# Kernel optimization log

Measured on AMD Instinct MI355X. Metric: run time of the kernel, lower is better.

## Reference

```python
import jax, jax.numpy as jnp
import numpy as np

B, C, T = 128, 23, 2000
N_FFT, HOP = 200, 100
NFREQ = N_FFT // 2 + 1        # 101
FT = 1 + (T - N_FFT) // HOP   # 19 time frames per channel
EMB, HEADS, DEPTH = 256, 8, 4
DH = EMB // HEADS             # 32 head dim
FF = 4 * EMB                  # 1024 ffn hidden
MASK_RATIO = 0.15


def _posenc(n, d):
    pos = np.arange(n)[:, None].astype(np.float32)
    div = np.exp(np.arange(0, d, 2).astype(np.float32) * -(np.log(10000.0) / d))
    pe = np.zeros((n, d), np.float32)
    pe[:, 0::2] = np.sin(pos * div)
    pe[:, 1::2] = np.cos(pos * div)
    return jnp.asarray(pe)


def _stft_mag(sig):
    # sig: (..., T) -> (..., FT, NFREQ); rectangular window, center=False, onesided
    idx = np.arange(FT)[:, None] * HOP + np.arange(N_FFT)[None, :]
    frames = sig[..., idx]                      # (..., FT, N_FFT)
    return jnp.abs(jnp.fft.rfft(frames, axis=-1))


def _layernorm(x, g, b):
    mu = x.mean(-1, keepdims=True)
    var = x.var(-1, keepdims=True)
    return (x - mu) / jnp.sqrt(var + 1e-5) * g + b


def setup_inputs() -> dict:
    key = jax.random.key(0)
    ks = jax.random.split(key, 12)
    inp = {
        'x': jax.random.normal(ks[0], (B, C, T), jnp.float32),
        'mask': jax.random.uniform(ks[1], (B, C, T)) < MASK_RATIO,
        'n_channel_offset': 0,
        'W_proj': jax.random.normal(ks[2], (NFREQ, EMB), jnp.float32) / np.sqrt(NFREQ),
        'b_proj': jnp.zeros((EMB,), jnp.float32),
        'channel_tokens': jax.random.normal(ks[3], (C, EMB), jnp.float32),
        'ln1_g': jnp.ones((DEPTH, EMB), jnp.float32),
        'ln1_b': jnp.zeros((DEPTH, EMB), jnp.float32),
        'Wq': jax.random.normal(ks[4], (DEPTH, EMB, EMB), jnp.float32) / np.sqrt(EMB),
        'Wk': jax.random.normal(ks[5], (DEPTH, EMB, EMB), jnp.float32) / np.sqrt(EMB),
        'Wv': jax.random.normal(ks[6], (DEPTH, EMB, EMB), jnp.float32) / np.sqrt(EMB),
        'Wo': jax.random.normal(ks[7], (DEPTH, EMB, EMB), jnp.float32) / np.sqrt(EMB),
        'ln2_g': jnp.ones((DEPTH, EMB), jnp.float32),
        'ln2_b': jnp.zeros((DEPTH, EMB), jnp.float32),
        'W1': jax.random.normal(ks[8], (DEPTH, EMB, FF), jnp.float32) / np.sqrt(EMB),
        'b1': jnp.zeros((DEPTH, FF), jnp.float32),
        'W2': jax.random.normal(ks[9], (DEPTH, FF, EMB), jnp.float32) / np.sqrt(FF),
        'b2': jnp.zeros((DEPTH, EMB), jnp.float32),
    }
    return inp


def reference(x, mask, n_channel_offset, W_proj, b_proj, channel_tokens,
              ln1_g, ln1_b, Wq, Wk, Wv, Wo, ln2_g, ln2_b, W1, b1, W2, b2):
    xm = jnp.where(mask, 0.0, x)
    # STFT magnitude for all channels at once: (B, C, FT, NFREQ)
    spec_c = _stft_mag(x)
    spec_m = _stft_mag(xm)
    # patch-frequency linear embedding -> (B, C, FT, EMB)
    emb_c = spec_c @ W_proj + b_proj
    emb_m = spec_m @ W_proj + b_proj
    tok = jnp.take(channel_tokens, jnp.arange(C) + n_channel_offset, axis=0)
    pe = _posenc(FT, EMB)
    emb_c = emb_c + tok[None, :, None, :] + pe[None, None, :, :]
    emb_m = emb_m + tok[None, :, None, :] + pe[None, None, :, :]
    S = C * FT
    emb_c = emb_c.reshape(B, S, EMB)
    h = emb_m.reshape(B, S, EMB)

    scale = DH ** -0.5
    for l in range(DEPTH):
        # linear attention block (prenorm)
        hn = _layernorm(h, ln1_g[l], ln1_b[l])
        q = (hn @ Wq[l]).reshape(B, S, HEADS, DH).transpose(0, 2, 1, 3)
        k = (hn @ Wk[l]).reshape(B, S, HEADS, DH).transpose(0, 2, 1, 3)
        v = (hn @ Wv[l]).reshape(B, S, HEADS, DH).transpose(0, 2, 1, 3)
        q = jax.nn.softmax(q, axis=-1) * scale   # softmax over feature dim
        k = jax.nn.softmax(k, axis=-2)           # softmax over sequence dim
        ctx = jnp.einsum('bhsd,bhse->bhde', k, v)      # (B,H,DH,DH)
        attn = jnp.einsum('bhsd,bhde->bhse', q, ctx)   # (B,H,S,DH)
        attn = attn.transpose(0, 2, 1, 3).reshape(B, S, EMB)
        h = h + attn @ Wo[l]
        # feed-forward block (prenorm)
        hn = _layernorm(h, ln2_g[l], ln2_b[l])
        h = h + jax.nn.gelu(hn @ W1[l] + b1[l]) @ W2[l] + b2[l]
    return (emb_c, h)
```

## Files before the change

kernel.cpp:

```cpp
#include <hip/hip_runtime.h>
#include <math.h>

#define BB 128
#define CC 23
#define TT 2000
#define NFFT 200
#define HOP 100
#define NFREQ 101
#define FTW 19
#define EMB 256
#define HEADS 8
#define DH 32
#define FFD 1024
#define DEPTH 4
#define SS (CC*FTW)
#define NROWS (BB*SS)
#define ROWT 16

typedef __attribute__((ext_vector_type(8))) short bf16x8;
typedef __attribute__((ext_vector_type(4))) float f32x4;
#define MFMA16 __builtin_amdgcn_mfma_f32_16x16x32_bf16

__device__ inline unsigned short f2bf(float f) {
    unsigned u = __float_as_uint(f);
    unsigned r = (u + 0x7FFFu + ((u >> 16) & 1u)) >> 16;
    return (unsigned short)r;
}
__device__ inline float bf2f(unsigned short s) {
    return __uint_as_float(((unsigned)s) << 16);
}
__device__ inline bf16x8 ld_frag(const unsigned short* p) {
    union { uint4 u; bf16x8 f; } v;
    v.u = *(const uint4*)p;
    return v.f;
}

__global__ __launch_bounds__(256) void k_init(float* pe) {
    int i = blockIdx.x * 256 + threadIdx.x;
    if (i < FTW * (EMB / 2)) {
        int t = i / (EMB / 2), j = i % (EMB / 2);
        float dv = expf((-9.210340371976184f / (float)EMB) * (float)(2 * j));
        float a = (float)t * dv;
        pe[t * EMB + 2 * j]     = sinf(a);
        pe[t * EMB + 2 * j + 1] = cosf(a);
    }
}

__global__ __launch_bounds__(256) void k_binit(unsigned short* Bt) {
    int i = blockIdx.x * 256 + threadIdx.x;
    if (i >= 256 * 224) return;
    int n = i / 224, k = i - (i / 224) * 224;
    int fq = ((n >> 5) << 4) + (n & 15);
    int kind = (n >> 4) & 1;
    float v = 0.f;
    if (k < 200 && fq < 101) {
        int kn = (fq * k) % 200;
        float th = 6.283185307179586f * (float)kn / 200.f;
        v = kind ? sinf(th) : cosf(th);
    }
    Bt[n * 224 + k] = f2bf(v);
}

__global__ __launch_bounds__(256) void k_tr(const float* __restrict__ in, unsigned short* __restrict__ out,
                                            int K, int N, size_t inStride, size_t outStride) {
    __shared__ float t[32][33];
    int k0 = blockIdx.y * 32, n0 = blockIdx.x * 32;
    const float* ip = in + blockIdx.z * inStride;
    unsigned short* op = out + blockIdx.z * outStride;
    int tx = threadIdx.x & 31, ty = threadIdx.x >> 5;
#pragma unroll
    for (int i = 0; i < 32; i += 8)
        t[ty + i][tx] = ip[(size_t)(k0 + ty + i) * N + n0 + tx];
    __syncthreads();
#pragma unroll
    for (int i = 0; i < 32; i += 8)
        op[(size_t)(n0 + ty + i) * K + k0 + tx] = f2bf(t[tx][ty + i]);
}

__global__ __launch_bounds__(256, 2) void k_stft(const float* __restrict__ x,
                                                 const int* __restrict__ mask,
                                                 const unsigned short* __restrict__ Bt,
                                                 float* __restrict__ specc,
                                                 float* __restrict__ specm) {
    int masked = blockIdx.y;
    int r0 = blockIdx.x * 64;
    __shared__ unsigned short aT[64 * 232];
    for (int t = threadIdx.x; t < 64 * 29; t += 256) {
        int row = t / 29;
        int ch = t - row * 29;
        int col0 = ch * 8;
        union { uint4 u; unsigned short s[8]; } pk;
        if (col0 < 200) {
            int fr = r0 + row;
            int bc = fr / 19, f = fr - bc * 19;
            const float* src = x + (size_t)bc * TT + f * HOP + col0;
            float4 v0 = *(const float4*)src;
            float4 v1 = *(const float4*)(src + 4);
            if (masked) {
                const int* ms = mask + (size_t)bc * TT + f * HOP + col0;
                int4 m0 = *(const int4*)ms;
                int4 m1 = *(const int4*)(ms + 4);
                if (m0.x) v0.x = 0.f; if (m0.y) v0.y = 0.f; if (m0.z) v0.z = 0.f; if (m0.w) v0.w = 0.f;
                if (m1.x) v1.x = 0.f; if (m1.y) v1.y = 0.f; if (m1.z) v1.z = 0.f; if (m1.w) v1.w = 0.f;
            }
            pk.s[0] = f2bf(v0.x); pk.s[1] = f2bf(v0.y); pk.s[2] = f2bf(v0.z); pk.s[3] = f2bf(v0.w);
            pk.s[4] = f2bf(v1.x); pk.s[5] = f2bf(v1.y); pk.s[6] = f2bf(v1.z); pk.s[7] = f2bf(v1.w);
        } else {
            pk.u = (uint4){0, 0, 0, 0};
        }
        *(uint4*)&aT[row * 232 + col0] = pk.u;
    }
    __syncthreads();
    int lane = threadIdx.x & 63, w = threadIdx.x >> 6;
    int m16 = lane & 15, q = lane >> 4;
    f32x4 acc[4][4];
#pragma unroll
    for (int mt = 0; mt < 4; mt++)
#pragma unroll
        for (int nt = 0; nt < 4; nt++) acc[mt][nt] = (f32x4){0.f, 0.f, 0.f, 0.f};
    for (int kk = 0; kk < 7; kk++) {
        int k0 = kk * 32 + q * 8;
        bf16x8 af[4], bfr[4];
#pragma unroll
        for (int mt = 0; mt < 4; mt++) af[mt] = ld_frag(&aT[(mt * 16 + m16) * 232 + k0]);
#pragma unroll
        for (int nt = 0; nt < 4; nt++) bfr[nt] = ld_frag(&Bt[(w * 64 + nt * 16 + m16) * 224 + k0]);
#pragma unroll
        for (int mt = 0; mt < 4; mt++)
#pragma unroll
            for (int nt = 0; nt < 4; nt++) acc[mt][nt] = MFMA16(af[mt], bfr[nt], acc[mt][nt], 0, 0, 0);
    }
    float* out = masked ? specm : specc;
#pragma unroll
    for (int pt = 0; pt < 2; pt++) {
        int fq = w * 32 + pt * 16 + m16;
        if (fq < NFREQ) {
#pragma unroll
            for (int mt = 0; mt < 4; mt++)
#pragma unroll
                for (int r = 0; r < 4; r++) {
                    float re = acc[mt][pt * 2][r];
                    float im = acc[mt][pt * 2 + 1][r];
                    int row = mt * 16 + q * 4 + r;
                    out[(size_t)(r0 + row) * NFREQ + fq] = sqrtf(re * re + im * im);
                }
        }
    }
}

__global__ __launch_bounds__(256) void k_proj(const float* __restrict__ spec,
                                              const float* __restrict__ Wp,
                                              const float* __restrict__ bp,
                                              const float* __restrict__ tok,
                                              const int* __restrict__ offp,
                                              const float* __restrict__ pe,
                                              float* __restrict__ out) {
    int r0 = blockIdx.x * ROWT;
    __shared__ float sp[ROWT][NFREQ];
    for (int i = threadIdx.x; i < ROWT * NFREQ; i += 256) {
        int r = i / NFREQ, kk = i % NFREQ;
        sp[r][kk] = spec[(size_t)(r0 + r) * NFREQ + kk];
    }
    __syncthreads();
    int j = threadIdx.x;
    float acc[ROWT];
#pragma unroll
    for (int r = 0; r < ROWT; r++) acc[r] = 0.f;
    for (int kk = 0; kk < NFREQ; kk++) {
        float w = Wp[kk * EMB + j];
#pragma unroll
        for (int r = 0; r < ROWT; r++) acc[r] += sp[r][kk] * w;
    }
    int off = *offp;
    float bj = bp[j];
#pragma unroll
    for (int r = 0; r < ROWT; r++) {
        int g = r0 + r;
        int c = (g / FTW) % CC;
        int f = g % FTW;
        out[(size_t)g * EMB + j] = acc[r] + bj + tok[(c + off) * EMB + j] + pe[f * EMB + j];
    }
}

__device__ inline void ln_stage8(const float* __restrict__ h, int r0,
                                 const float* __restrict__ g, const float* __restrict__ b,
                                 unsigned short* aT) {
    int row = threadIdx.x >> 3, part = threadIdx.x & 7;
    const float* hr = h + (size_t)(r0 + row) * EMB + part * 32;
    float s1 = 0.f, s2 = 0.f;
#pragma unroll
    for (int i = 0; i < 8; i++) {
        float4 v = *(const float4*)(hr + i * 4);
        s1 += v.x + v.y + v.z + v.w;
        s2 += v.x * v.x + v.y * v.y + v.z * v.z + v.w * v.w;
    }
    s1 += __shfl_xor(s1, 1); s1 += __shfl_xor(s1, 2); s1 += __shfl_xor(s1, 4);
    s2 += __shfl_xor(s2, 1); s2 += __shfl_xor(s2, 2); s2 += __shfl_xor(s2, 4);
    float mu = s1 * (1.f / EMB);
    float var = s2 * (1.f / EMB) - mu * mu;
    float rstd = rsqrtf(var + 1e-5f);
    const float* gp = g + part * 32;
    const float* bp = b + part * 32;
#pragma unroll
    for (int i = 0; i < 4; i++) {
        float4 va = *(const float4*)(hr + i * 8);
        float4 vb = *(const float4*)(hr + i * 8 + 4);
        float4 ga = *(const float4*)(gp + i * 8);
        float4 gb = *(const float4*)(gp + i * 8 + 4);
        float4 ba = *(const float4*)(bp + i * 8);
        float4 bb = *(const float4*)(bp + i * 8 + 4);
        union { uint4 u; unsigned short s[8]; } pk;
        pk.s[0] = f2bf((va.x - mu) * rstd * ga.x + ba.x);
        pk.s[1] = f2bf((va.y - mu) * rstd * ga.y + ba.y);
        pk.s[2] = f2bf((va.z - mu) * rstd * ga.z + ba.z);
        pk.s[3] = f2bf((va.w - mu) * rstd * ga.w + ba.w);
        pk.s[4] = f2bf((vb.x - mu) * rstd * gb.x + bb.x);
        pk.s[5] = f2bf((vb.y - mu) * rstd * gb.y + bb.y);
        pk.s[6] = f2bf((vb.z - mu) * rstd * gb.z + bb.z);
        pk.s[7] = f2bf((vb.w - mu) * rstd * gb.w + bb.w);
        *(uint4*)&aT[row * 264 + part * 32 + i * 8] = pk.u;
    }
}

__global__ __launch_bounds__(512, 4) void k_qkv(const float* __restrict__ h,
                                                const float* __restrict__ lng,
                                                const float* __restrict__ lnb,
                                                const unsigned short* __restrict__ Wt,
                                                unsigned short* __restrict__ qb,
                                                unsigned short* __restrict__ kb,
                                                unsigned short* __restrict__ vb) {
    __shared__ unsigned short aT[64 * 264];
    __shared__ unsigned short ob[64 * 264];
    int r0 = blockIdx.x * 64;
    ln_stage8(h, r0, lng, lnb, aT);
    __syncthreads();
    int lane = threadIdx.x & 63, w = threadIdx.x >> 6;
    int m16 = lane & 15, q = lane >> 4;
    f32x4 acc[4][2];

    auto do_gemm = [&](int gg) {
        int cb = gg * 256 + w * 32;
#pragma unroll
        for (int mt = 0; mt < 4; mt++)
#pragma unroll
            for (int nt = 0; nt < 2; nt++) acc[mt][nt] = (f32x4){0.f, 0.f, 0.f, 0.f};
        bf16x8 bc0 = ld_frag(&Wt[(size_t)(cb + m16) * EMB + q * 8]);
        bf16x8 bc1 = ld_frag(&Wt[(size_t)(cb + 16 + m16) * EMB + q * 8]);
        for (int kk = 0; kk < 8; kk++) {
            int k0 = kk * 32 + q * 8;
            bf16x8 bn0, bn1;
            if (kk < 7) {
                bn0 = ld_frag(&Wt[(size_t)(cb + m16) * EMB + k0 + 32]);
                bn1 = ld_frag(&Wt[(size_t)(cb + 16 + m16) * EMB + k0 + 32]);
            }
            bf16x8 af[4];
#pragma unroll
            for (int mt = 0; mt < 4; mt++) af[mt] = ld_frag(&aT[(mt * 16 + m16) * 264 + k0]);
#pragma unroll
            for (int mt = 0; mt < 4; mt++) acc[mt][0] = MFMA16(af[mt], bc0, acc[mt][0], 0, 0, 0);
#pragma unroll
            for (int mt = 0; mt < 4; mt++) acc[mt][1] = MFMA16(af[mt], bc1, acc[mt][1], 0, 0, 0);
            bc0 = bn0; bc1 = bn1;
        }
    };

    do_gemm(0);
    for (int gg = 0; gg < 3; gg++) {
        __syncthreads();
#pragma unroll
        for (int nt = 0; nt < 2; nt++)
#pragma unroll
            for (int mt = 0; mt < 4; mt++)
#pragma unroll
                for (int r = 0; r < 4; r++)
                    ob[(mt * 16 + q * 4 + r) * 264 + w * 32 + nt * 16 + m16] = f2bf(acc[mt][nt][r]);
        __syncthreads();
        unsigned short* dst = (gg == 0) ? qb : (gg == 1) ? kb : vb;
        for (int t = threadIdx.x; t < 2048; t += 512) {
            int row = t >> 5, c8 = (t & 31) * 8;
            *(uint4*)&dst[(size_t)(r0 + row) * EMB + c8] = *(uint4*)&ob[row * 264 + c8];
        }
        if (gg < 2) do_gemm(gg + 1);
    }
}

__global__ __launch_bounds__(256) void k_kctx(const unsigned short* __restrict__ kb,
                                              const unsigned short* __restrict__ vb,
                                              float* __restrict__ ctx) {
    int b = blockIdx.x >> 3, h = blockIdx.x & 7;
    int d = threadIdx.x & 31, g = threadIdx.x >> 5;
    size_t colbase = (size_t)b * SS * EMB + h * DH;
    __shared__ float red[8][32];
    __shared__ float kmax[32], krs[32];
    float mx = -1e30f;
    for (int s = g; s < SS; s += 8) mx = fmaxf(mx, bf2f(kb[colbase + (size_t)s * EMB + d]));
    red[g][d] = mx;
    __syncthreads();
    if (threadIdx.x < 32) {
        mx = red[0][d];
        for (int i = 1; i < 8; i++) mx = fmaxf(mx, red[i][d]);
        kmax[d] = mx;
    }
    __syncthreads();
    mx = kmax[d];
    float sm = 0.f;
    for (int s = g; s < SS; s += 8) sm += __expf(bf2f(kb[colbase + (size_t)s * EMB + d]) - mx);
    __syncthreads();
    red[g][d] = sm;
    __syncthreads();
    if (threadIdx.x < 32) {
        sm = 0.f;
        for (int i = 0; i < 8; i++) sm += red[i][d];
        krs[d] = 1.f / sm;
    }
    __syncthreads();
    int e = threadIdx.x & 31, db = threadIdx.x >> 5;
    float acc[4] = {0.f, 0.f, 0.f, 0.f};
    __shared__ float ksm[8][32], vls[8][32];
    float kmd = kmax[d], krd = krs[d];
    for (int s0 = 0; s0 < SS; s0 += 8) {
        int s = s0 + g;
        float kvv = 0.f, vvv = 0.f;
        if (s < SS) {
            kvv = __expf(bf2f(kb[colbase + (size_t)s * EMB + d]) - kmd) * krd;
            vvv = bf2f(vb[colbase + (size_t)s * EMB + d]);
        }
        __syncthreads();
        ksm[g][d] = kvv;
        vls[g][d] = vvv;
        __syncthreads();
#pragma unroll
        for (int ssx = 0; ssx < 8; ssx++) {
            float vv = vls[ssx][e];
#pragma unroll
            for (int i = 0; i < 4; i++) acc[i] += ksm[ssx][db * 4 + i] * vv;
        }
    }
#pragma unroll
    for (int i = 0; i < 4; i++)
        ctx[((size_t)b * HEADS + h) * 1024 + e * 32 + (db * 4 + i)] = acc[i];
}

__global__ __launch_bounds__(256, 4) void k_attn_o(const unsigned short* __restrict__ qb,
                                                   const float* __restrict__ ctxT,
                                                   const unsigned short* __restrict__ WoT,
                                                   float* __restrict__ h) {
    int b = blockIdx.x, s0 = blockIdx.y * 16;
    __shared__ unsigned short qsmb[16 * 264];
    __shared__ unsigned short ctxb[8 * 32 * 48];
    __shared__ unsigned short atb[16 * 264];
    int j = threadIdx.x;
    for (int idx = j; idx < 8192; idx += 256) {
        int hh = idx >> 10, rem = idx & 1023, e = rem >> 5, d = rem & 31;
        ctxb[hh * (32 * 48) + e * 48 + d] = f2bf(ctxT[(size_t)b * 8192 + idx]);
    }
    const float scale = 0.17677669529663687f;
    for (int r = 0; r < 16; r++) {
        int s = s0 + r; if (s > SS - 1) s = SS - 1;
        float v = bf2f(qb[((size_t)b * SS + s) * EMB + j]);
        float mxv = v;
#pragma unroll
        for (int m = 1; m < 32; m <<= 1) mxv = fmaxf(mxv, __shfl_xor(mxv, m));
        float ex = __expf(v - mxv);
        float sm = ex;
#pragma unroll
        for (int m = 1; m < 32; m <<= 1) sm += __shfl_xor(sm, m);
        qsmb[r * 264 + j] = f2bf(ex / sm * scale);
    }
    __syncthreads();
    int lane = threadIdx.x & 63, w = threadIdx.x >> 6;
    int m16 = lane & 15, q = lane >> 4;
#pragma unroll
    for (int hi = 0; hi < 2; hi++) {
        int head = w * 2 + hi;
        bf16x8 af = ld_frag(&qsmb[m16 * 264 + head * 32 + q * 8]);
#pragma unroll
        for (int half = 0; half < 2; half++) {
            bf16x8 bfr = ld_frag(&ctxb[head * (32 * 48) + (half * 16 + m16) * 48 + q * 8]);
            f32x4 acc = (f32x4){0.f, 0.f, 0.f, 0.f};
            acc = MFMA16(af, bfr, acc, 0, 0, 0);
#pragma unroll
            for (int r = 0; r < 4; r++)
                atb[(q * 4 + r) * 264 + head * 32 + half * 16 + m16] = f2bf(acc[r]);
        }
    }
    __syncthreads();
    f32x4 acc2[4];
#pragma unroll
    for (int nt = 0; nt < 4; nt++) acc2[nt] = (f32x4){0.f, 0.f, 0.f, 0.f};
    for (int kk = 0; kk < 8; kk++) {
        int k0 = kk * 32 + q * 8;
        bf16x8 af = ld_frag(&atb[m16 * 264 + k0]);
#pragma unroll
        for (int nt = 0; nt < 4; nt++) {
            bf16x8 bfr = ld_frag(&WoT[(size_t)(w * 64 + nt * 16 + m16) * EMB + k0]);
            acc2[nt] = MFMA16(af, bfr, acc2[nt], 0, 0, 0);
        }
    }
#pragma unroll
    for (int nt = 0; nt < 4; nt++) {
        int c = w * 64 + nt * 16 + m16;
#pragma unroll
        for (int r = 0; r < 4; r++) {
            int s = s0 + q * 4 + r;
            if (s < SS) h[((size_t)b * SS + s) * EMB + c] += acc2[nt][r];
        }
    }
}

__global__ __launch_bounds__(512, 4) void k_ffn(const float* __restrict__ hin,
                                                const float* __restrict__ lng,
                                                const float* __restrict__ lnb,
                                                const unsigned short* __restrict__ W1T,
                                                const float* __restrict__ b1,
                                                const unsigned short* __restrict__ W2T,
                                                const float* __restrict__ b2,
                                                float* __restrict__ h) {
    __shared__ unsigned short aT[64 * 264];
    __shared__ unsigned short fch[64 * 264];
    int r0 = blockIdx.x * 64;
    ln_stage8(hin, r0, lng, lnb, aT);
    __syncthreads();
    int lane = threadIdx.x & 63, w = threadIdx.x >> 6;
    int m16 = lane & 15, q = lane >> 4;
    f32x4 acc2[4][2];
#pragma unroll
    for (int mt = 0; mt < 4; mt++)
#pragma unroll
        for (int nt = 0; nt < 2; nt++) acc2[mt][nt] = (f32x4){0.f, 0.f, 0.f, 0.f};
    f32x4 accf[4][2];

    auto gemm1 = [&](int ch) {
        int cb = ch * 256 + w * 32;
#pragma unroll
        for (int mt = 0; mt < 4; mt++)
#pragma unroll
            for (int nt = 0; nt < 2; nt++) accf[mt][nt] = (f32x4){0.f, 0.f, 0.f, 0.f};
        bf16x8 bc0 = ld_frag(&W1T[(size_t)(cb + m16) * EMB + q * 8]);
        bf16x8 bc1 = ld_frag(&W1T[(size_t)(cb + 16 + m16) * EMB + q * 8]);
        for (int kk = 0; kk < 8; kk++) {
            int k0 = kk * 32 + q * 8;
            bf16x8 bn0, bn1;
            if (kk < 7) {
                bn0 = ld_frag(&W1T[(size_t)(cb + m16) * EMB + k0 + 32]);
                bn1 = ld_frag(&W1T[(size_t)(cb + 16 + m16) * EMB + k0 + 32]);
            }
            bf16x8 af[4];
#pragma unroll
            for (int mt = 0; mt < 4; mt++) af[mt] = ld_frag(&aT[(mt * 16 + m16) * 264 + k0]);
#pragma unroll
            for (int mt = 0; mt < 4; mt++) accf[mt][0] = MFMA16(af[mt], bc0, accf[mt][0], 0, 0, 0);
#pragma unroll
            for (int mt = 0; mt < 4; mt++) accf[mt][1] = MFMA16(af[mt], bc1, accf[mt][1], 0, 0, 0);
            bc0 = bn0; bc1 = bn1;
        }
    };

    gemm1(0);
    for (int ch = 0; ch < 4; ch++) {
        __syncthreads();
#pragma unroll
        for (int nt = 0; nt < 2; nt++) {
            int cl = w * 32 + nt * 16 + m16;
            float bias = b1[ch * 256 + cl];
#pragma unroll
            for (int mt = 0; mt < 4; mt++)
#pragma unroll
                for (int r = 0; r < 4; r++) {
                    float xv = accf[mt][nt][r] + bias;
                    float z = 0.7978845608028654f * (xv + 0.044715f * xv * xv * xv);
                    z = fminf(fmaxf(z, -15.f), 15.f);
                    float t = __expf(2.f * z);
                    float gl = 0.5f * xv * (1.f + (t - 1.f) / (t + 1.f));
                    fch[(mt * 16 + q * 4 + r) * 264 + cl] = f2bf(gl);
                }
        }
        __syncthreads();
        {
            int rb = w * 32;
            bf16x8 bc0 = ld_frag(&W2T[(size_t)(rb + m16) * FFD + ch * 256 + q * 8]);
            bf16x8 bc1 = ld_frag(&W2T[(size_t)(rb + 16 + m16) * FFD + ch * 256 + q * 8]);
            for (int kk = 0; kk < 8; kk++) {
                int k0 = kk * 32 + q * 8;
                bf16x8 bn0, bn1;
                if (kk < 7) {
                    bn0 = ld_frag(&W2T[(size_t)(rb + m16) * FFD + ch * 256 + k0 + 32]);
                    bn1 = ld_frag(&W2T[(size_t)(rb + 16 + m16) * FFD + ch * 256 + k0 + 32]);
                }
                bf16x8 af[4];
#pragma unroll
                for (int mt = 0; mt < 4; mt++) af[mt] = ld_frag(&fch[(mt * 16 + m16) * 264 + k0]);
#pragma unroll
                for (int mt = 0; mt < 4; mt++) acc2[mt][0] = MFMA16(af[mt], bc0, acc2[mt][0], 0, 0, 0);
#pragma unroll
                for (int mt = 0; mt < 4; mt++) acc2[mt][1] = MFMA16(af[mt], bc1, acc2[mt][1], 0, 0, 0);
                bc0 = bn0; bc1 = bn1;
            }
        }
        if (ch < 3) gemm1(ch + 1);
    }
#pragma unroll
    for (int nt = 0; nt < 2; nt++) {
        int c = w * 32 + nt * 16 + m16;
        float bias = b2[c];
#pragma unroll
        for (int mt = 0; mt < 4; mt++)
#pragma unroll
            for (int r = 0; r < 4; r++)
                h[(size_t)(r0 + mt * 16 + q * 4 + r) * EMB + c] += acc2[mt][nt][r] + bias;
    }
}

extern "C" void kernel_launch(void* const* d_in, const int* in_sizes, int n_in,
                              void* d_out, int out_size, void* d_ws, size_t ws_size,
                              hipStream_t stream) {
    const float* x    = (const float*)d_in[0];
    const int* mask   = (const int*)d_in[1];
    const int* offp   = (const int*)d_in[2];
    const float* Wp   = (const float*)d_in[3];
    const float* bp   = (const float*)d_in[4];
    const float* tok  = (const float*)d_in[5];
    const float* ln1g = (const float*)d_in[6];
    const float* ln1b = (const float*)d_in[7];
    const float* Wq   = (const float*)d_in[8];
    const float* Wk   = (const float*)d_in[9];
    const float* Wv   = (const float*)d_in[10];
    const float* Wo   = (const float*)d_in[11];
    const float* ln2g = (const float*)d_in[12];
    const float* ln2b = (const float*)d_in[13];
    const float* W1   = (const float*)d_in[14];
    const float* b1   = (const float*)d_in[15];
    const float* W2   = (const float*)d_in[16];
    const float* b2   = (const float*)d_in[17];

    float* out_embc = (float*)d_out;
    float* h = out_embc + (size_t)NROWS * EMB;

    char* base = (char*)d_ws;
    float* pe = (float*)base;
    unsigned short* Bt = (unsigned short*)(base + 19712);
    unsigned short* wT = (unsigned short*)(base + 134400);
    unsigned short* qb = (unsigned short*)(base + 6425856);
    unsigned short* kb = qb + (size_t)NROWS * EMB;
    unsigned short* vb = kb + (size_t)NROWS * EMB;
    float* specc = (float*)qb;
    float* specm = specc + (size_t)NROWS * NFREQ;
    float* ctxT = (float*)(base + 6425856 + 3ull * NROWS * EMB * 2);

    unsigned short* WqkvT = wT;
    unsigned short* WoT   = wT + 786432;
    unsigned short* W1T   = WoT + 262144;
    unsigned short* W2T   = W1T + 1048576;

    k_init<<<10, 256, 0, stream>>>(pe);
    k_binit<<<224, 256, 0, stream>>>(Bt);
    k_tr<<<dim3(8, 8, 4), 256, 0, stream>>>(Wq, WqkvT + 0,      256, 256, 65536, 196608);
    k_tr<<<dim3(8, 8, 4), 256, 0, stream>>>(Wk, WqkvT + 65536,  256, 256, 65536, 196608);
    k_tr<<<dim3(8, 8, 4), 256, 0, stream>>>(Wv, WqkvT + 131072, 256, 256, 65536, 196608);
    k_tr<<<dim3(8, 8, 4), 256, 0, stream>>>(Wo, WoT, 256, 256, 65536, 65536);
    k_tr<<<dim3(32, 8, 4), 256, 0, stream>>>(W1, W1T, 256, 1024, 262144, 262144);
    k_tr<<<dim3(8, 32, 4), 256, 0, stream>>>(W2, W2T, 1024, 256, 262144, 262144);

    k_stft<<<dim3(NROWS / 64, 2), 256, 0, stream>>>(x, mask, Bt, specc, specm);
    k_proj<<<NROWS / ROWT, 256, 0, stream>>>(specc, Wp, bp, tok, offp, pe, out_embc);
    k_proj<<<NROWS / ROWT, 256, 0, stream>>>(specm, Wp, bp, tok, offp, pe, h);

    for (int l = 0; l < DEPTH; l++) {
        k_qkv<<<NROWS / 64, 512, 0, stream>>>(h, ln1g + l * EMB, ln1b + l * EMB,
                                              WqkvT + (size_t)l * 196608, qb, kb, vb);
        k_kctx<<<BB * HEADS, 256, 0, stream>>>(kb, vb, ctxT);
        k_attn_o<<<dim3(BB, (SS + 15) / 16), 256, 0, stream>>>(qb, ctxT, WoT + (size_t)l * 65536, h);
        k_ffn<<<NROWS / 64, 512, 0, stream>>>(h, ln2g + l * EMB, ln2b + l * EMB,
                                              W1T + (size_t)l * 262144, b1 + (size_t)l * FFD,
                                              W2T + (size_t)l * 262144, b2 + (size_t)l * EMB, h);
    }
}
```

Before: 2.153 ms.

## Halve chunk width in QKV and FFN kernels to cut LDS and registers

The QKV and FFN kernels now process output columns in 128-wide chunks instead of 256-wide ones. That halves the staging LDS buffer and the per-wave accumulator registers, and launch bounds are raised from 4 to 6 blocks per CU so more blocks can be resident. The activation row stride is also padded from 264 to 280 to change the LDS bank mapping. The cost is twice as many sync/epilogue rounds, and each B fragment is reused across fewer MFMAs, so global weight loads per FLOP go up.

```diff
diff --git a/kernel.cpp b/kernel.cpp
--- a/kernel.cpp
+++ b/kernel.cpp
@@ -16,6 +16,8 @@
 #define SS (CC*FTW)
 #define NROWS (BB*SS)
 #define ROWT 16
+#define ATS 280
+#define FCS 136
 
 typedef __attribute__((ext_vector_type(8))) short bf16x8;
 typedef __attribute__((ext_vector_type(4))) float f32x4;
@@ -218,69 +220,60 @@
         pk.s[5] = f2bf((vb.y - mu) * rstd * gb.y + bb.y);
         pk.s[6] = f2bf((vb.z - mu) * rstd * gb.z + bb.z);
         pk.s[7] = f2bf((vb.w - mu) * rstd * gb.w + bb.w);
-        *(uint4*)&aT[row * 264 + part * 32 + i * 8] = pk.u;
-    }
-}
-
-__global__ __launch_bounds__(512, 4) void k_qkv(const float* __restrict__ h,
+        *(uint4*)&aT[row * ATS + part * 32 + i * 8] = pk.u;
+    }
+}
+
+__global__ __launch_bounds__(512, 6) void k_qkv(const float* __restrict__ h,
                                                 const float* __restrict__ lng,
                                                 const float* __restrict__ lnb,
                                                 const unsigned short* __restrict__ Wt,
                                                 unsigned short* __restrict__ qb,
                                                 unsigned short* __restrict__ kb,
                                                 unsigned short* __restrict__ vb) {
-    __shared__ unsigned short aT[64 * 264];
-    __shared__ unsigned short ob[64 * 264];
+    __shared__ unsigned short aT[64 * ATS];
+    __shared__ unsigned short ob[64 * FCS];
     int r0 = blockIdx.x * 64;
     ln_stage8(h, r0, lng, lnb, aT);
     __syncthreads();
     int lane = threadIdx.x & 63, w = threadIdx.x >> 6;
     int m16 = lane & 15, q = lane >> 4;
-    f32x4 acc[4][2];
+    f32x4 acc[4];
 
     auto do_gemm = [&](int gg) {
-        int cb = gg * 256 + w * 32;
-#pragma unroll
-        for (int mt = 0; mt < 4; mt++)
-#pragma unroll
-            for (int nt = 0; nt < 2; nt++) acc[mt][nt] = (f32x4){0.f, 0.f, 0.f, 0.f};
-        bf16x8 bc0 = ld_frag(&Wt[(size_t)(cb + m16) * EMB + q * 8]);
-        bf16x8 bc1 = ld_frag(&Wt[(size_t)(cb + 16 + m16) * EMB + q * 8]);
+        int cb = gg * 128 + w * 16;
+#pragma unroll
+        for (int mt = 0; mt < 4; mt++) acc[mt] = (f32x4){0.f, 0.f, 0.f, 0.f};
+        bf16x8 bc = ld_frag(&Wt[(size_t)(cb + m16) * EMB + q * 8]);
         for (int kk = 0; kk < 8; kk++) {
             int k0 = kk * 32 + q * 8;
-            bf16x8 bn0, bn1;
-            if (kk < 7) {
-                bn0 = ld_frag(&Wt[(size_t)(cb + m16) * EMB + k0 + 32]);
-                bn1 = ld_frag(&Wt[(size_t)(cb + 16 + m16) * EMB + k0 + 32]);
-            }
+            bf16x8 bn;
+            if (kk < 7) bn = ld_frag(&Wt[(size_t)(cb + m16) * EMB + k0 + 32]);
             bf16x8 af[4];
 #pragma unroll
-            for (int mt = 0; mt < 4; mt++) af[mt] = ld_frag(&aT[(mt * 16 + m16) * 264 + k0]);
-#pragma unroll
-            for (int mt = 0; mt < 4; mt++) acc[mt][0] = MFMA16(af[mt], bc0, acc[mt][0], 0, 0, 0);
-#pragma unroll
-            for (int mt = 0; mt < 4; mt++) acc[mt][1] = MFMA16(af[mt], bc1, acc[mt][1], 0, 0, 0);
-            bc0 = bn0; bc1 = bn1;
+            for (int mt = 0; mt < 4; mt++) af[mt] = ld_frag(&aT[(mt * 16 + m16) * ATS + k0]);
+#pragma unroll
+            for (int mt = 0; mt < 4; mt++) acc[mt] = MFMA16(af[mt], bc, acc[mt], 0, 0, 0);
+            bc = bn;
         }
     };
 
     do_gemm(0);
-    for (int gg = 0; gg < 3; gg++) {
+    for (int gg = 0; gg < 6; gg++) {
         __syncthreads();
 #pragma unroll
-        for (int nt = 0; nt < 2; nt++)
-#pragma unroll
-            for (int mt = 0; mt < 4; mt++)
-#pragma unroll
-                for (int r = 0; r < 4; r++)
-                    ob[(mt * 16 + q * 4 + r) * 264 + w * 32 + nt * 16 + m16] = f2bf(acc[mt][nt][r]);
+        for (int mt = 0; mt < 4; mt++)
+#pragma unroll
+            for (int r = 0; r < 4; r++)
+                ob[(mt * 16 + q * 4 + r) * FCS + w * 16 + m16] = f2bf(acc[mt][r]);
         __syncthreads();
-        unsigned short* dst = (gg == 0) ? qb : (gg == 1) ? kb : vb;
-        for (int t = threadIdx.x; t < 2048; t += 512) {
-            int row = t >> 5, c8 = (t & 31) * 8;
-            *(uint4*)&dst[(size_t)(r0 + row) * EMB + c8] = *(uint4*)&ob[row * 264 + c8];
-        }
-        if (gg < 2) do_gemm(gg + 1);
+        unsigned short* dst = (gg < 2) ? qb : (gg < 4) ? kb : vb;
+        int cc0 = (gg & 1) * 128;
+        for (int t = threadIdx.x; t < 1024; t += 512) {
+            int row = t >> 4, c8 = (t & 15) * 8;
+            *(uint4*)&dst[(size_t)(r0 + row) * EMB + cc0 + c8] = *(uint4*)&ob[row * FCS + c8];
+        }
+        if (gg < 5) do_gemm(gg + 1);
     }
 }
 
@@ -408,7 +401,7 @@
     }
 }
 
-__global__ __launch_bounds__(512, 4) void k_ffn(const float* __restrict__ hin,
+__global__ __launch_bounds__(512, 6) void k_ffn(const float* __restrict__ hin,
                                                 const float* __restrict__ lng,
                                                 const float* __restrict__ lnb,
                                                 const unsigned short* __restrict__ W1T,
@@ -416,8 +409,8 @@
                                                 const unsigned short* __restrict__ W2T,
                                                 const float* __restrict__ b2,
                                                 float* __restrict__ h) {
-    __shared__ unsigned short aT[64 * 264];
-    __shared__ unsigned short fch[64 * 264];
+    __shared__ unsigned short aT[64 * ATS];
+    __shared__ unsigned short fch[64 * FCS];
     int r0 = blockIdx.x * 64;
     ln_stage8(hin, r0, lng, lnb, aT);
     __syncthreads();
@@ -428,68 +421,58 @@
     for (int mt = 0; mt < 4; mt++)
 #pragma unroll
         for (int nt = 0; nt < 2; nt++) acc2[mt][nt] = (f32x4){0.f, 0.f, 0.f, 0.f};
-    f32x4 accf[4][2];
+    f32x4 acc1[4];
 
     auto gemm1 = [&](int ch) {
-        int cb = ch * 256 + w * 32;
-#pragma unroll
-        for (int mt = 0; mt < 4; mt++)
-#pragma unroll
-            for (int nt = 0; nt < 2; nt++) accf[mt][nt] = (f32x4){0.f, 0.f, 0.f, 0.f};
-        bf16x8 bc0 = ld_frag(&W1T[(size_t)(cb + m16) * EMB + q * 8]);
-        bf16x8 bc1 = ld_frag(&W1T[(size_t)(cb + 16 + m16) * EMB + q * 8]);
+        int cb = ch * 128 + w * 16;
+#pragma unroll
+        for (int mt = 0; mt < 4; mt++) acc1[mt] = (f32x4){0.f, 0.f, 0.f, 0.f};
+        bf16x8 bc = ld_frag(&W1T[(size_t)(cb + m16) * EMB + q * 8]);
         for (int kk = 0; kk < 8; kk++) {
             int k0 = kk * 32 + q * 8;
-            bf16x8 bn0, bn1;
-            if (kk < 7) {
-                bn0 = ld_frag(&W1T[(size_t)(cb + m16) * EMB + k0 + 32]);
-                bn1 = ld_frag(&W1T[(size_t)(cb + 16 + m16) * EMB + k0 + 32]);
-            }
+            bf16x8 bn;
+            if (kk < 7) bn = ld_frag(&W1T[(size_t)(cb + m16) * EMB + k0 + 32]);
             bf16x8 af[4];
 #pragma unroll
-            for (int mt = 0; mt < 4; mt++) af[mt] = ld_frag(&aT[(mt * 16 + m16) * 264 + k0]);
-#pragma unroll
-            for (int mt = 0; mt < 4; mt++) accf[mt][0] = MFMA16(af[mt], bc0, accf[mt][0], 0, 0, 0);
-#pragma unroll
-            for (int mt = 0; mt < 4; mt++) accf[mt][1] = MFMA16(af[mt], bc1, accf[mt][1], 0, 0, 0);
-            bc0 = bn0; bc1 = bn1;
+            for (int mt = 0; mt < 4; mt++) af[mt] = ld_frag(&aT[(mt * 16 + m16) * ATS + k0]);
+#pragma unroll
+            for (int mt = 0; mt < 4; mt++) acc1[mt] = MFMA16(af[mt], bc, acc1[mt], 0, 0, 0);
+            bc = bn;
         }
     };
 
     gemm1(0);
-    for (int ch = 0; ch < 4; ch++) {
+    for (int ch = 0; ch < 8; ch++) {
         __syncthreads();
-#pragma unroll
-        for (int nt = 0; nt < 2; nt++) {
-            int cl = w * 32 + nt * 16 + m16;
-            float bias = b1[ch * 256 + cl];
+        {
+            float bias = b1[ch * 128 + w * 16 + m16];
 #pragma unroll
             for (int mt = 0; mt < 4; mt++)
 #pragma unroll
                 for (int r = 0; r < 4; r++) {
-                    float xv = accf[mt][nt][r] + bias;
+                    float xv = acc1[mt][r] + bias;
                     float z = 0.7978845608028654f * (xv + 0.044715f * xv * xv * xv);
                     z = fminf(fmaxf(z, -15.f), 15.f);
                     float t = __expf(2.f * z);
                     float gl = 0.5f * xv * (1.f + (t - 1.f) / (t + 1.f));
-                    fch[(mt * 16 + q * 4 + r) * 264 + cl] = f2bf(gl);
+                    fch[(mt * 16 + q * 4 + r) * FCS + w * 16 + m16] = f2bf(gl);
                 }
         }
         __syncthreads();
         {
             int rb = w * 32;
-            bf16x8 bc0 = ld_frag(&W2T[(size_t)(rb + m16) * FFD + ch * 256 + q * 8]);
-            bf16x8 bc1 = ld_frag(&W2T[(size_t)(rb + 16 + m16) * FFD + ch * 256 + q * 8]);
-            for (int kk = 0; kk < 8; kk++) {
+            bf16x8 bc0 = ld_frag(&W2T[(size_t)(rb + m16) * FFD + ch * 128 + q * 8]);
+            bf16x8 bc1 = ld_frag(&W2T[(size_t)(rb + 16 + m16) * FFD + ch * 128 + q * 8]);
+            for (int kk = 0; kk < 4; kk++) {
                 int k0 = kk * 32 + q * 8;
                 bf16x8 bn0, bn1;
-                if (kk < 7) {
-                    bn0 = ld_frag(&W2T[(size_t)(rb + m16) * FFD + ch * 256 + k0 + 32]);
-                    bn1 = ld_frag(&W2T[(size_t)(rb + 16 + m16) * FFD + ch * 256 + k0 + 32]);
+                if (kk < 3) {
+                    bn0 = ld_frag(&W2T[(size_t)(rb + m16) * FFD + ch * 128 + k0 + 32]);
+                    bn1 = ld_frag(&W2T[(size_t)(rb + 16 + m16) * FFD + ch * 128 + k0 + 32]);
                 }
                 bf16x8 af[4];
 #pragma unroll
-                for (int mt = 0; mt < 4; mt++) af[mt] = ld_frag(&fch[(mt * 16 + m16) * 264 + k0]);
+                for (int mt = 0; mt < 4; mt++) af[mt] = ld_frag(&fch[(mt * 16 + m16) * FCS + k0]);
 #pragma unroll
                 for (int mt = 0; mt < 4; mt++) acc2[mt][0] = MFMA16(af[mt], bc0, acc2[mt][0], 0, 0, 0);
 #pragma unroll
@@ -497,7 +480,7 @@
                 bc0 = bn0; bc1 = bn1;
             }
         }
-        if (ch < 3) gemm1(ch + 1);
+        if (ch < 7) gemm1(ch + 1);
     }
 #pragma unroll
     for (int nt = 0; nt < 2; nt++) {
```

Result: slower. 2.342 ms (+8.8%).

## Retile FFN kernel to 32-row blocks with 128-wide hidden chunks

Applied to the files above, without the earlier changes.

The fused FFN kernel now processes 32 rows per block with 256 threads instead of 64 rows with 512. The hidden dimension is handled in eight 128-wide chunks, and each wave owns 64 output columns in the second GEMM. This shrinks shared memory per block and doubles the grid size, aiming for better occupancy and latency hiding. The cost is that W1/W2 weights are re-read by twice as many blocks, and there is more MFMA work per A-fragment load and less per B-fragment load. Named stride constants are introduced for the LDS row pitches.

```diff
diff --git a/kernel.cpp b/kernel.cpp
--- a/kernel.cpp
+++ b/kernel.cpp
@@ -16,6 +16,8 @@
 #define SS (CC*FTW)
 #define NROWS (BB*SS)
 #define ROWT 16
+#define ATS 264
+#define FCS 136
 
 typedef __attribute__((ext_vector_type(8))) short bf16x8;
 typedef __attribute__((ext_vector_type(4))) float f32x4;
@@ -218,7 +220,7 @@
         pk.s[5] = f2bf((vb.y - mu) * rstd * gb.y + bb.y);
         pk.s[6] = f2bf((vb.z - mu) * rstd * gb.z + bb.z);
         pk.s[7] = f2bf((vb.w - mu) * rstd * gb.w + bb.w);
-        *(uint4*)&aT[row * 264 + part * 32 + i * 8] = pk.u;
+        *(uint4*)&aT[row * ATS + part * 32 + i * 8] = pk.u;
     }
 }
 
@@ -229,8 +231,8 @@
                                                 unsigned short* __restrict__ qb,
                                                 unsigned short* __restrict__ kb,
                                                 unsigned short* __restrict__ vb) {
-    __shared__ unsigned short aT[64 * 264];
-    __shared__ unsigned short ob[64 * 264];
+    __shared__ unsigned short aT[64 * ATS];
+    __shared__ unsigned short ob[64 * ATS];
     int r0 = blockIdx.x * 64;
     ln_stage8(h, r0, lng, lnb, aT);
     __syncthreads();
@@ -255,7 +257,7 @@
             }
             bf16x8 af[4];
 #pragma unroll
-            for (int mt = 0; mt < 4; mt++) af[mt] = ld_frag(&aT[(mt * 16 + m16) * 264 + k0]);
+            for (int mt = 0; mt < 4; mt++) af[mt] = ld_frag(&aT[(mt * 16 + m16) * ATS + k0]);
 #pragma unroll
             for (int mt = 0; mt < 4; mt++) acc[mt][0] = MFMA16(af[mt], bc0, acc[mt][0], 0, 0, 0);
 #pragma unroll
@@ -273,12 +275,12 @@
             for (int mt = 0; mt < 4; mt++)
 #pragma unroll
                 for (int r = 0; r < 4; r++)
-                    ob[(mt * 16 + q * 4 + r) * 264 + w * 32 + nt * 16 + m16] = f2bf(acc[mt][nt][r]);
+                    ob[(mt * 16 + q * 4 + r) * ATS + w * 32 + nt * 16 + m16] = f2bf(acc[mt][nt][r]);
         __syncthreads();
         unsigned short* dst = (gg == 0) ? qb : (gg == 1) ? kb : vb;
         for (int t = threadIdx.x; t < 2048; t += 512) {
             int row = t >> 5, c8 = (t & 31) * 8;
-            *(uint4*)&dst[(size_t)(r0 + row) * EMB + c8] = *(uint4*)&ob[row * 264 + c8];
+            *(uint4*)&dst[(size_t)(r0 + row) * EMB + c8] = *(uint4*)&ob[row * ATS + c8];
         }
         if (gg < 2) do_gemm(gg + 1);
     }
@@ -408,7 +410,7 @@
     }
 }
 
-__global__ __launch_bounds__(512, 4) void k_ffn(const float* __restrict__ hin,
+__global__ __launch_bounds__(256, 4) void k_ffn(const float* __restrict__ hin,
                                                 const float* __restrict__ lng,
                                                 const float* __restrict__ lnb,
                                                 const unsigned short* __restrict__ W1T,
@@ -416,26 +418,26 @@
                                                 const unsigned short* __restrict__ W2T,
                                                 const float* __restrict__ b2,
                                                 float* __restrict__ h) {
-    __shared__ unsigned short aT[64 * 264];
-    __shared__ unsigned short fch[64 * 264];
-    int r0 = blockIdx.x * 64;
+    __shared__ unsigned short aT[32 * ATS];
+    __shared__ unsigned short fch[32 * FCS];
+    int r0 = blockIdx.x * 32;
     ln_stage8(hin, r0, lng, lnb, aT);
     __syncthreads();
     int lane = threadIdx.x & 63, w = threadIdx.x >> 6;
     int m16 = lane & 15, q = lane >> 4;
-    f32x4 acc2[4][2];
-#pragma unroll
-    for (int mt = 0; mt < 4; mt++)
-#pragma unroll
-        for (int nt = 0; nt < 2; nt++) acc2[mt][nt] = (f32x4){0.f, 0.f, 0.f, 0.f};
-    f32x4 accf[4][2];
+    f32x4 acc2[2][4];
+#pragma unroll
+    for (int mt = 0; mt < 2; mt++)
+#pragma unroll
+        for (int nt = 0; nt < 4; nt++) acc2[mt][nt] = (f32x4){0.f, 0.f, 0.f, 0.f};
+    f32x4 acc1[2][2];
 
     auto gemm1 = [&](int ch) {
-        int cb = ch * 256 + w * 32;
-#pragma unroll
-        for (int mt = 0; mt < 4; mt++)
-#pragma unroll
-            for (int nt = 0; nt < 2; nt++) accf[mt][nt] = (f32x4){0.f, 0.f, 0.f, 0.f};
+        int cb = ch * 128 + w * 32;
+#pragma unroll
+        for (int mt = 0; mt < 2; mt++)
+#pragma unroll
+            for (int nt = 0; nt < 2; nt++) acc1[mt][nt] = (f32x4){0.f, 0.f, 0.f, 0.f};
         bf16x8 bc0 = ld_frag(&W1T[(size_t)(cb + m16) * EMB + q * 8]);
         bf16x8 bc1 = ld_frag(&W1T[(size_t)(cb + 16 + m16) * EMB + q * 8]);
         for (int kk = 0; kk < 8; kk++) {
@@ -445,66 +447,70 @@
                 bn0 = ld_frag(&W1T[(size_t)(cb + m16) * EMB + k0 + 32]);
                 bn1 = ld_frag(&W1T[(size_t)(cb + 16 + m16) * EMB + k0 + 32]);
             }
-            bf16x8 af[4];
-#pragma unroll
-            for (int mt = 0; mt < 4; mt++) af[mt] = ld_frag(&aT[(mt * 16 + m16) * 264 + k0]);
-#pragma unroll
-            for (int mt = 0; mt < 4; mt++) accf[mt][0] = MFMA16(af[mt], bc0, accf[mt][0], 0, 0, 0);
-#pragma unroll
-            for (int mt = 0; mt < 4; mt++) accf[mt][1] = MFMA16(af[mt], bc1, accf[mt][1], 0, 0, 0);
+            bf16x8 af[2];
+#pragma unroll
+            for (int mt = 0; mt < 2; mt++) af[mt] = ld_frag(&aT[(mt * 16 + m16) * ATS + k0]);
+#pragma unroll
+            for (int mt = 0; mt < 2; mt++) acc1[mt][0] = MFMA16(af[mt], bc0, acc1[mt][0], 0, 0, 0);
+#pragma unroll
+            for (int mt = 0; mt < 2; mt++) acc1[mt][1] = MFMA16(af[mt], bc1, acc1[mt][1], 0, 0, 0);
             bc0 = bn0; bc1 = bn1;
         }
     };
 
     gemm1(0);
-    for (int ch = 0; ch < 4; ch++) {
+    for (int ch = 0; ch < 8; ch++) {
         __syncthreads();
 #pragma unroll
         for (int nt = 0; nt < 2; nt++) {
             int cl = w * 32 + nt * 16 + m16;
-            float bias = b1[ch * 256 + cl];
-#pragma unroll
-            for (int mt = 0; mt < 4; mt++)
+            float bias = b1[ch * 128 + cl];
+#pragma unroll
+            for (int mt = 0; mt < 2; mt++)
 #pragma unroll
                 for (int r = 0; r < 4; r++) {
-                    float xv = accf[mt][nt][r] + bias;
+                    float xv = acc1[mt][nt][r] + bias;
                     float z = 0.7978845608028654f * (xv + 0.044715f * xv * xv * xv);
                     z = fminf(fmaxf(z, -15.f), 15.f);
                     float t = __expf(2.f * z);
                     float gl = 0.5f * xv * (1.f + (t - 1.f) / (t + 1.f));
-                    fch[(mt * 16 + q * 4 + r) * 264 + cl] = f2bf(gl);
+                    fch[(mt * 16 + q * 4 + r) * FCS + cl] = f2bf(gl);
                 }
         }
         __syncthreads();
         {
-            int rb = w * 32;
-            bf16x8 bc0 = ld_frag(&W2T[(size_t)(rb + m16) * FFD + ch * 256 + q * 8]);
-            bf16x8 bc1 = ld_frag(&W2T[(size_t)(rb + 16 + m16) * FFD + ch * 256 + q * 8]);
-            for (int kk = 0; kk < 8; kk++) {
+            int rb = w * 64;
+            bf16x8 bc[4];
+#pragma unroll
+            for (int nt = 0; nt < 4; nt++)
+                bc[nt] = ld_frag(&W2T[(size_t)(rb + nt * 16 + m16) * FFD + ch * 128 + q * 8]);
+            for (int kk = 0; kk < 4; kk++) {
                 int k0 = kk * 32 + q * 8;
-                bf16x8 bn0, bn1;
-                if (kk < 7) {
-                    bn0 = ld_frag(&W2T[(size_t)(rb + m16) * FFD + ch * 256 + k0 + 32]);
-                    bn1 = ld_frag(&W2T[(size_t)(rb + 16 + m16) * FFD + ch * 256 + k0 + 32]);
+                bf16x8 bn[4];
+                if (kk < 3) {
+#pragma unroll
+                    for (int nt = 0; nt < 4; nt++)
+                        bn[nt] = ld_frag(&W2T[(size_t)(rb + nt * 16 + m16) * FFD + ch * 128 + k0 + 32]);
                 }
-                bf16x8 af[4];
-#pragma unroll
-                for (int mt = 0; mt < 4; mt++) af[mt] = ld_frag(&fch[(mt * 16 + m16) * 264 + k0]);
-#pragma unroll
-                for (int mt = 0; mt < 4; mt++) acc2[mt][0] = MFMA16(af[mt], bc0, acc2[mt][0], 0, 0, 0);
-#pragma unroll
-                for (int mt = 0; mt < 4; mt++) acc2[mt][1] = MFMA16(af[mt], bc1, acc2[mt][1], 0, 0, 0);
-                bc0 = bn0; bc1 = bn1;
+                bf16x8 af[2];
+#pragma unroll
+                for (int mt = 0; mt < 2; mt++) af[mt] = ld_frag(&fch[(mt * 16 + m16) * FCS + k0]);
+#pragma unroll
+                for (int nt = 0; nt < 4; nt++)
+#pragma unroll
+                    for (int mt = 0; mt < 2; mt++) acc2[mt][nt] = MFMA16(af[mt], bc[nt], acc2[mt][nt], 0, 0, 0);
+#pragma unroll
+                for (int nt = 0; nt < 4; nt++) bc[nt] = bn[nt];
             }
         }
-        if (ch < 3) gemm1(ch + 1);
-    }
-#pragma unroll
-    for (int nt = 0; nt < 2; nt++) {
-        int c = w * 32 + nt * 16 + m16;
+        if (ch < 7) gemm1(ch + 1);
+    }
+#pragma unroll
+    for (int nt = 0; nt < 4; nt++) {
+        int c = w * 64 + nt * 16 + m16;
         float bias = b2[c];
 #pragma unroll
-        for (int mt = 0; mt < 4; mt++)
+        for (int mt = 0; mt < 2; mt++)
 #pragma unroll
             for (int r = 0; r < 4; r++)
                 h[(size_t)(r0 + mt * 16 + q * 4 + r) * EMB + c] += acc2[mt][nt][r] + bias;
@@ -570,7 +576,7 @@
                                               WqkvT + (size_t)l * 196608, qb, kb, vb);
         k_kctx<<<BB * HEADS, 256, 0, stream>>>(kb, vb, ctxT);
         k_attn_o<<<dim3(BB, (SS + 15) / 16), 256, 0, stream>>>(qb, ctxT, WoT + (size_t)l * 65536, h);
-        k_ffn<<<NROWS / 64, 512, 0, stream>>>(h, ln2g + l * EMB, ln2b + l * EMB,
+        k_ffn<<<NROWS / 32, 256, 0, stream>>>(h, ln2g + l * EMB, ln2b + l * EMB,
                                               W1T + (size_t)l * 262144, b1 + (size_t)l * FFD,
                                               W2T + (size_t)l * 262144, b2 + (size_t)l * EMB, h);
     }
```

Result: slower. 2.409 ms (+11.9%).
